# Optimization experiments

Hardware: AMD Instinct MI355X
Metric: run time of the kernel (lower is better)

Reference implementation:

```python
import jax, jax.numpy as jnp
import numpy as np

N_BITS = 8
QMAX = 2 ** (N_BITS - 1) - 1  # 127 for int8 symmetric
EPS = 1e-8


def fake_quant(x, axis):
    """Symmetric per-slice (row/col) dynamic fake quantization with STE-compatible form."""
    amax = jnp.max(jnp.abs(x), axis=axis, keepdims=True)
    scale = jnp.maximum(amax, EPS) / QMAX
    q = jnp.clip(jnp.round(x / scale), -QMAX - 1, QMAX) * scale
    return q


def setup_inputs() -> dict:
    key = jax.random.key(0)
    k1, k2 = jax.random.split(key)
    inputs1 = jax.random.normal(k1, (2, 16, 2048, 128), dtype=jnp.float32)
    inputs2 = jax.random.normal(k2, (2, 16, 128, 2048), dtype=jnp.float32)
    return {"inputs1": inputs1, "inputs2": inputs2}


def reference(inputs1, inputs2):
    # input1: row-wise (axes=-1) quant; input2: axes=-1 (module default); output: row-wise
    q1 = fake_quant(inputs1, axis=-1)
    q2 = fake_quant(inputs2, axis=-1)
    out = jnp.matmul(q1, q2)  # [B, H, S, S]
    return fake_quant(out, axis=-1)
```

## Files before the change

### kernel.cpp

```cpp
#include <hip/hip_runtime.h>
#include <hip/hip_bf16.h>
#include <cstdint>

#define QMAXF 127.0f
#define EPSQ 1e-8f

typedef __bf16 bf16x8 __attribute__((ext_vector_type(8)));
typedef float f32x4 __attribute__((ext_vector_type(4)));

static constexpr int BB = 32;
static constexpr int MM = 2048;
static constexpr int KK = 128;
static constexpr int NN = 2048;

static constexpr size_t OFF_Q1   = 0;
static constexpr size_t OFF_Q2T  = OFF_Q1  + (size_t)BB*MM*KK*2;
static constexpr size_t OFF_S1   = OFF_Q2T + (size_t)BB*NN*KK*2;
static constexpr size_t OFF_S2   = OFF_S1  + (size_t)BB*MM*4;

__global__ __launch_bounds__(256) void quant_rows128(const float* __restrict__ x,
                                                     unsigned short* __restrict__ q,
                                                     float* __restrict__ s1) {
    int wave = threadIdx.x >> 6, lane = threadIdx.x & 63;
    int row = blockIdx.x * 4 + wave;
    const float2* xr = reinterpret_cast<const float2*>(x) + (size_t)row * 64;
    float2 v = xr[lane];
    float a = fmaxf(fabsf(v.x), fabsf(v.y));
#pragma unroll
    for (int m = 32; m; m >>= 1) a = fmaxf(a, __shfl_xor(a, m));
    float scale = fmaxf(a, EPSQ) / QMAXF;
    float i0 = fminf(fmaxf(rintf(v.x / scale), -128.f), 127.f);
    float i1 = fminf(fmaxf(rintf(v.y / scale), -128.f), 127.f);
    __bf16 h0 = (__bf16)i0, h1 = (__bf16)i1;
    ushort2 st;
    st.x = *reinterpret_cast<unsigned short*>(&h0);
    st.y = *reinterpret_cast<unsigned short*>(&h1);
    reinterpret_cast<ushort2*>(q + (size_t)row * 128)[lane ^ ((row & 7) << 2)] = st;
    if (lane == 0) s1[row] = scale;
}

__global__ __launch_bounds__(256) void amax_rows2048(const float* __restrict__ x,
                                                     float* __restrict__ s2) {
    int row = blockIdx.x;
    const float4* xr = reinterpret_cast<const float4*>(x) + (size_t)row * 512;
    int t = threadIdx.x;
    float4 v0 = xr[t], v1 = xr[t + 256];
    float a = fmaxf(fmaxf(fmaxf(fabsf(v0.x), fabsf(v0.y)), fmaxf(fabsf(v0.z), fabsf(v0.w))),
                    fmaxf(fmaxf(fabsf(v1.x), fabsf(v1.y)), fmaxf(fabsf(v1.z), fabsf(v1.w))));
#pragma unroll
    for (int m = 32; m; m >>= 1) a = fmaxf(a, __shfl_xor(a, m));
    __shared__ float red[4];
    if ((t & 63) == 0) red[t >> 6] = a;
    __syncthreads();
    if (t == 0) {
        float m0 = fmaxf(fmaxf(red[0], red[1]), fmaxf(red[2], red[3]));
        s2[row] = fmaxf(m0, EPSQ) / QMAXF;
    }
}

__global__ __launch_bounds__(256) void quant_transpose(const float* __restrict__ x,
                                                       const float* __restrict__ s2,
                                                       unsigned short* __restrict__ q2t) {
    int b = blockIdx.x >> 5;
    int n0 = (blockIdx.x & 31) * 64;
    __shared__ unsigned short lds[64][136];
    int t = threadIdx.x;
    int rr = t >> 4, cc = t & 15;
#pragma unroll
    for (int p = 0; p < 8; ++p) {
        int k = p * 16 + rr;
        float s = s2[b * 128 + k];
        const float4* src = reinterpret_cast<const float4*>(x + ((size_t)b * 128 + k) * 2048 + n0);
        float4 v = src[cc];
        float f[4] = {v.x, v.y, v.z, v.w};
#pragma unroll
        for (int e = 0; e < 4; ++e) {
            float iq = fminf(fmaxf(rintf(f[e] / s), -128.f), 127.f);
            __bf16 h = (__bf16)(iq * s);
            lds[cc * 4 + e][k] = *reinterpret_cast<unsigned short*>(&h);
        }
    }
    __syncthreads();
    int nl = t >> 2, seg = t & 3;
    int sw = nl & 7;
    uint4* dstrow = reinterpret_cast<uint4*>(q2t + ((size_t)b * 2048 + n0 + nl) * 128);
#pragma unroll
    for (int j = 0; j < 4; ++j)
        dstrow[(seg * 4 + j) ^ sw] = *reinterpret_cast<const uint4*>(&lds[nl][seg * 32 + j * 8]);
}

__global__ __launch_bounds__(256, 2) void gemm_fused(const unsigned short* __restrict__ qa,
                                                     const unsigned short* __restrict__ qbt,
                                                     const float* __restrict__ s1,
                                                     float* __restrict__ out) {
    int id = blockIdx.x;
    int nid = (id & 7) * 64 + (id >> 3);
    int b = nid >> 4, mt = nid & 15;

    __shared__ float rowAmax[128], sOsc[128], sQs[128], sS1[128];

    int tid = threadIdx.x, wave = tid >> 6, lane = tid & 63;
    if (tid < 128) {
        rowAmax[tid] = 0.f;
        sS1[tid] = s1[b * 2048 + mt * 128 + tid];
    }

    int wm = wave >> 1, wn = wave & 1;
    int lr = lane & 15, lg = lane >> 4;
    int swz = (lr & 7) << 3;

    bf16x8 afr[4][4];
    {
        const unsigned short* Ai = qa + (size_t)(b * 16 + mt) * 16384;
#pragma unroll
        for (int ks = 0; ks < 4; ++ks)
#pragma unroll
            for (int mi = 0; mi < 4; ++mi)
                afr[ks][mi] = *reinterpret_cast<const bf16x8*>(
                    &Ai[(wm * 64 + mi * 16 + lr) * 128 + ((ks * 32 + lg * 8) ^ swz)]);
    }

    const unsigned short* Bimg = qbt + (size_t)b * 16 * 16384;
    auto boff = [&](int nt, int ks, int ni) -> size_t {
        return (size_t)(nt * 128 + wn * 64 + ni * 16 + lr) * 128 + ((ks * 32 + lg * 8) ^ swz);
    };

    bf16x8 bfr[4][4];
#pragma unroll
    for (int ks = 0; ks < 4; ++ks)
#pragma unroll
        for (int ni = 0; ni < 4; ++ni)
            bfr[ks][ni] = *reinterpret_cast<const bf16x8*>(&Bimg[boff(0, ks, ni)]);

    size_t ob = (size_t)b * 2048 * 2048;
    float rmax[4] = {0.f, 0.f, 0.f, 0.f};

    for (int nt = 0; nt < 16; ++nt) {
        int nn = (nt + 1) & 15;
        f32x4 acc[4][4];
#pragma unroll
        for (int mi = 0; mi < 4; ++mi)
#pragma unroll
            for (int ni = 0; ni < 4; ++ni) {
                f32x4 z = {0.f, 0.f, 0.f, 0.f};
                acc[mi][ni] = z;
            }
#pragma unroll
        for (int ks = 0; ks < 4; ++ks) {
#pragma unroll
            for (int mi = 0; mi < 4; ++mi)
#pragma unroll
                for (int ni = 0; ni < 4; ++ni)
                    acc[mi][ni] = __builtin_amdgcn_mfma_f32_16x16x32_bf16(bfr[ks][ni], afr[ks][mi], acc[mi][ni], 0, 0, 0);
#pragma unroll
            for (int ni = 0; ni < 4; ++ni)
                bfr[ks][ni] = *reinterpret_cast<const bf16x8*>(&Bimg[boff(nn, ks, ni)]);
        }
#pragma unroll
        for (int mi = 0; mi < 4; ++mi)
#pragma unroll
            for (int ni = 0; ni < 4; ++ni)
#pragma unroll
                for (int r = 0; r < 4; ++r)
                    rmax[mi] = fmaxf(rmax[mi], fabsf(acc[mi][ni][r]));
    }

#pragma unroll
    for (int mi = 0; mi < 4; ++mi) {
        float v = rmax[mi];
        v = fmaxf(v, __shfl_xor(v, 16));
        v = fmaxf(v, __shfl_xor(v, 32));
        if (lg == 0) {
            int row = wm * 64 + mi * 16 + lr;
            atomicMax(reinterpret_cast<unsigned*>(&rowAmax[row]), __float_as_uint(v));
        }
    }
    __syncthreads();
    if (tid < 128) {
        float am = rowAmax[tid] * sS1[tid];
        float osc = fmaxf(am, EPSQ) / QMAXF;
        sOsc[tid] = osc;
        sQs[tid] = sS1[tid] / osc;
    }
    __syncthreads();

    for (int nt = 0; nt < 16; ++nt) {
        int nn = (nt + 1) & 15;
        f32x4 acc[4][4];
#pragma unroll
        for (int mi = 0; mi < 4; ++mi)
#pragma unroll
            for (int ni = 0; ni < 4; ++ni) {
                f32x4 z = {0.f, 0.f, 0.f, 0.f};
                acc[mi][ni] = z;
            }
#pragma unroll
        for (int ks = 0; ks < 4; ++ks) {
#pragma unroll
            for (int mi = 0; mi < 4; ++mi)
#pragma unroll
                for (int ni = 0; ni < 4; ++ni)
                    acc[mi][ni] = __builtin_amdgcn_mfma_f32_16x16x32_bf16(bfr[ks][ni], afr[ks][mi], acc[mi][ni], 0, 0, 0);
#pragma unroll
            for (int ni = 0; ni < 4; ++ni)
                bfr[ks][ni] = *reinterpret_cast<const bf16x8*>(&Bimg[boff(nn, ks, ni)]);
        }
#pragma unroll
        for (int mi = 0; mi < 4; ++mi) {
            int row = wm * 64 + mi * 16 + lr;
            float qs = sQs[row], osc = sOsc[row];
            size_t rowoff = ob + (size_t)(mt * 128 + row) * 2048 + nt * 128 + wn * 64 + lg * 4;
#pragma unroll
            for (int ni = 0; ni < 4; ++ni) {
                f32x4 qv;
                qv[0] = fminf(fmaxf(rintf(acc[mi][ni][0] * qs), -128.f), 127.f) * osc;
                qv[1] = fminf(fmaxf(rintf(acc[mi][ni][1] * qs), -128.f), 127.f) * osc;
                qv[2] = fminf(fmaxf(rintf(acc[mi][ni][2] * qs), -128.f), 127.f) * osc;
                qv[3] = fminf(fmaxf(rintf(acc[mi][ni][3] * qs), -128.f), 127.f) * osc;
                *reinterpret_cast<f32x4*>(&out[rowoff + ni * 16]) = qv;
            }
        }
    }
}

extern "C" void kernel_launch(void* const* d_in, const int* in_sizes, int n_in,
                              void* d_out, int out_size, void* d_ws, size_t ws_size,
                              hipStream_t stream) {
    const float* in1 = (const float*)d_in[0];
    const float* in2 = (const float*)d_in[1];
    char* ws = (char*)d_ws;
    unsigned short* q1  = (unsigned short*)(ws + OFF_Q1);
    unsigned short* q2t = (unsigned short*)(ws + OFF_Q2T);
    float* s1   = (float*)(ws + OFF_S1);
    float* s2   = (float*)(ws + OFF_S2);
    float* out  = (float*)d_out;

    quant_rows128 <<<BB * MM / 4, 256, 0, stream>>>(in1, q1, s1);
    amax_rows2048 <<<BB * KK,     256, 0, stream>>>(in2, s2);
    quant_transpose<<<BB * (NN / 64), 256, 0, stream>>>(in2, s2, q2t);
    gemm_fused    <<<BB * 16,     256, 0, stream>>>(q1, q2t, s1, out);
}
```

Before: 191.8 us.

## Re-tile fused GEMM so each wave covers all 128 rows and prefetches B four tiles ahead

Changes the fused quantized GEMM's wave decomposition. Each wave now holds A fragments for all 128 rows and one 16-column strip per 64-column step, instead of a 64x64 quadrant. B is loaded through four rotating register banks, so each load is issued four sub-tiles ahead to hide global-load latency. The per-row scale and inverse are packed into one float2 in LDS. The cost is doubled A-fragment registers and narrower per-wave output writes (16 columns per store group), which may cost occupancy or store coalescing.

```diff
diff --git a/kernel.cpp b/kernel.cpp
--- a/kernel.cpp
+++ b/kernel.cpp
@@ -97,129 +97,121 @@
     int nid = (id & 7) * 64 + (id >> 3);
     int b = nid >> 4, mt = nid & 15;
 
-    __shared__ float rowAmax[128], sOsc[128], sQs[128], sS1[128];
+    __shared__ float rowAmax[128], sS1[128];
+    __shared__ float2 sQO[128];
 
     int tid = threadIdx.x, wave = tid >> 6, lane = tid & 63;
     if (tid < 128) {
         rowAmax[tid] = 0.f;
         sS1[tid] = s1[b * 2048 + mt * 128 + tid];
     }
-
-    int wm = wave >> 1, wn = wave & 1;
+    __syncthreads();
+
     int lr = lane & 15, lg = lane >> 4;
     int swz = (lr & 7) << 3;
 
-    bf16x8 afr[4][4];
+    bf16x8 afr[4][8];
     {
         const unsigned short* Ai = qa + (size_t)(b * 16 + mt) * 16384;
 #pragma unroll
         for (int ks = 0; ks < 4; ++ks)
 #pragma unroll
-            for (int mi = 0; mi < 4; ++mi)
+            for (int mi = 0; mi < 8; ++mi)
                 afr[ks][mi] = *reinterpret_cast<const bf16x8*>(
-                    &Ai[(wm * 64 + mi * 16 + lr) * 128 + ((ks * 32 + lg * 8) ^ swz)]);
+                    &Ai[(mi * 16 + lr) * 128 + ((ks * 32 + lg * 8) ^ swz)]);
     }
 
     const unsigned short* Bimg = qbt + (size_t)b * 16 * 16384;
-    auto boff = [&](int nt, int ks, int ni) -> size_t {
-        return (size_t)(nt * 128 + wn * 64 + ni * 16 + lr) * 128 + ((ks * 32 + lg * 8) ^ swz);
+    auto boff = [&](int t64, int ks) -> size_t {
+        return (size_t)(t64 * 64 + wave * 16 + lr) * 128 + ((ks * 32 + lg * 8) ^ swz);
     };
 
-    bf16x8 bfr[4][4];
-#pragma unroll
-    for (int ks = 0; ks < 4; ++ks)
-#pragma unroll
-        for (int ni = 0; ni < 4; ++ni)
-            bfr[ks][ni] = *reinterpret_cast<const bf16x8*>(&Bimg[boff(0, ks, ni)]);
+    bf16x8 bk0[4], bk1[4], bk2[4], bk3[4];
+#pragma unroll
+    for (int ks = 0; ks < 4; ++ks) {
+        bk0[ks] = *reinterpret_cast<const bf16x8*>(&Bimg[boff(0, ks)]);
+        bk1[ks] = *reinterpret_cast<const bf16x8*>(&Bimg[boff(1, ks)]);
+        bk2[ks] = *reinterpret_cast<const bf16x8*>(&Bimg[boff(2, ks)]);
+        bk3[ks] = *reinterpret_cast<const bf16x8*>(&Bimg[boff(3, ks)]);
+    }
 
     size_t ob = (size_t)b * 2048 * 2048;
-    float rmax[4] = {0.f, 0.f, 0.f, 0.f};
-
-    for (int nt = 0; nt < 16; ++nt) {
-        int nn = (nt + 1) & 15;
-        f32x4 acc[4][4];
-#pragma unroll
-        for (int mi = 0; mi < 4; ++mi)
-#pragma unroll
-            for (int ni = 0; ni < 4; ++ni) {
-                f32x4 z = {0.f, 0.f, 0.f, 0.f};
-                acc[mi][ni] = z;
-            }
+    float rmax[8];
+#pragma unroll
+    for (int mi = 0; mi < 8; ++mi) rmax[mi] = 0.f;
+
+    auto s1body = [&](int t, bf16x8 (&bank)[4]) {
+        f32x4 acc[8];
+#pragma unroll
+        for (int mi = 0; mi < 8; ++mi) { f32x4 z = {0.f,0.f,0.f,0.f}; acc[mi] = z; }
+        int nn = (t + 4) & 31;
 #pragma unroll
         for (int ks = 0; ks < 4; ++ks) {
 #pragma unroll
-            for (int mi = 0; mi < 4; ++mi)
-#pragma unroll
-                for (int ni = 0; ni < 4; ++ni)
-                    acc[mi][ni] = __builtin_amdgcn_mfma_f32_16x16x32_bf16(bfr[ks][ni], afr[ks][mi], acc[mi][ni], 0, 0, 0);
-#pragma unroll
-            for (int ni = 0; ni < 4; ++ni)
-                bfr[ks][ni] = *reinterpret_cast<const bf16x8*>(&Bimg[boff(nn, ks, ni)]);
-        }
-#pragma unroll
-        for (int mi = 0; mi < 4; ++mi)
-#pragma unroll
-            for (int ni = 0; ni < 4; ++ni)
-#pragma unroll
-                for (int r = 0; r < 4; ++r)
-                    rmax[mi] = fmaxf(rmax[mi], fabsf(acc[mi][ni][r]));
-    }
-
-#pragma unroll
-    for (int mi = 0; mi < 4; ++mi) {
+            for (int mi = 0; mi < 8; ++mi)
+                acc[mi] = __builtin_amdgcn_mfma_f32_16x16x32_bf16(bank[ks], afr[ks][mi], acc[mi], 0, 0, 0);
+            bank[ks] = *reinterpret_cast<const bf16x8*>(&Bimg[boff(nn, ks)]);
+        }
+#pragma unroll
+        for (int mi = 0; mi < 8; ++mi)
+#pragma unroll
+            for (int r = 0; r < 4; ++r)
+                rmax[mi] = fmaxf(rmax[mi], fabsf(acc[mi][r]));
+    };
+    for (int t = 0; t < 32; t += 4) {
+        s1body(t + 0, bk0);
+        s1body(t + 1, bk1);
+        s1body(t + 2, bk2);
+        s1body(t + 3, bk3);
+    }
+
+#pragma unroll
+    for (int mi = 0; mi < 8; ++mi) {
         float v = rmax[mi];
         v = fmaxf(v, __shfl_xor(v, 16));
         v = fmaxf(v, __shfl_xor(v, 32));
         if (lg == 0) {
-            int row = wm * 64 + mi * 16 + lr;
-            atomicMax(reinterpret_cast<unsigned*>(&rowAmax[row]), __float_as_uint(v));
+            atomicMax(reinterpret_cast<unsigned*>(&rowAmax[mi * 16 + lr]), __float_as_uint(v));
         }
     }
     __syncthreads();
     if (tid < 128) {
         float am = rowAmax[tid] * sS1[tid];
         float osc = fmaxf(am, EPSQ) / QMAXF;
-        sOsc[tid] = osc;
-        sQs[tid] = sS1[tid] / osc;
-    }
-    __syncthreads();
-
-    for (int nt = 0; nt < 16; ++nt) {
-        int nn = (nt + 1) & 15;
-        f32x4 acc[4][4];
-#pragma unroll
-        for (int mi = 0; mi < 4; ++mi)
-#pragma unroll
-            for (int ni = 0; ni < 4; ++ni) {
-                f32x4 z = {0.f, 0.f, 0.f, 0.f};
-                acc[mi][ni] = z;
-            }
+        sQO[tid] = make_float2(sS1[tid] / osc, osc);
+    }
+    __syncthreads();
+
+    auto s2body = [&](int t, bf16x8 (&bank)[4]) {
+        f32x4 acc[8];
+#pragma unroll
+        for (int mi = 0; mi < 8; ++mi) { f32x4 z = {0.f,0.f,0.f,0.f}; acc[mi] = z; }
+        int nn = (t + 4) & 31;
 #pragma unroll
         for (int ks = 0; ks < 4; ++ks) {
 #pragma unroll
-            for (int mi = 0; mi < 4; ++mi)
-#pragma unroll
-                for (int ni = 0; ni < 4; ++ni)
-                    acc[mi][ni] = __builtin_amdgcn_mfma_f32_16x16x32_bf16(bfr[ks][ni], afr[ks][mi], acc[mi][ni], 0, 0, 0);
-#pragma unroll
-            for (int ni = 0; ni < 4; ++ni)
-                bfr[ks][ni] = *reinterpret_cast<const bf16x8*>(&Bimg[boff(nn, ks, ni)]);
-        }
-#pragma unroll
-        for (int mi = 0; mi < 4; ++mi) {
-            int row = wm * 64 + mi * 16 + lr;
-            float qs = sQs[row], osc = sOsc[row];
-            size_t rowoff = ob + (size_t)(mt * 128 + row) * 2048 + nt * 128 + wn * 64 + lg * 4;
-#pragma unroll
-            for (int ni = 0; ni < 4; ++ni) {
-                f32x4 qv;
-                qv[0] = fminf(fmaxf(rintf(acc[mi][ni][0] * qs), -128.f), 127.f) * osc;
-                qv[1] = fminf(fmaxf(rintf(acc[mi][ni][1] * qs), -128.f), 127.f) * osc;
-                qv[2] = fminf(fmaxf(rintf(acc[mi][ni][2] * qs), -128.f), 127.f) * osc;
-                qv[3] = fminf(fmaxf(rintf(acc[mi][ni][3] * qs), -128.f), 127.f) * osc;
-                *reinterpret_cast<f32x4*>(&out[rowoff + ni * 16]) = qv;
-            }
-        }
+            for (int mi = 0; mi < 8; ++mi)
+                acc[mi] = __builtin_amdgcn_mfma_f32_16x16x32_bf16(bank[ks], afr[ks][mi], acc[mi], 0, 0, 0);
+            bank[ks] = *reinterpret_cast<const bf16x8*>(&Bimg[boff(nn, ks)]);
+        }
+#pragma unroll
+        for (int mi = 0; mi < 8; ++mi) {
+            int row = mi * 16 + lr;
+            float2 qo = sQO[row];
+            f32x4 qv;
+            qv[0] = fminf(fmaxf(rintf(acc[mi][0] * qo.x), -128.f), 127.f) * qo.y;
+            qv[1] = fminf(fmaxf(rintf(acc[mi][1] * qo.x), -128.f), 127.f) * qo.y;
+            qv[2] = fminf(fmaxf(rintf(acc[mi][2] * qo.x), -128.f), 127.f) * qo.y;
+            qv[3] = fminf(fmaxf(rintf(acc[mi][3] * qo.x), -128.f), 127.f) * qo.y;
+            *reinterpret_cast<f32x4*>(
+                &out[ob + (size_t)(mt * 128 + row) * 2048 + t * 64 + wave * 16 + lg * 4]) = qv;
+        }
+    };
+    for (int t = 0; t < 32; t += 4) {
+        s2body(t + 0, bk0);
+        s2body(t + 1, bk1);
+        s2body(t + 2, bk2);
+        s2body(t + 3, bk3);
     }
 }
 
```

New measurement: 535.7 us. +179.2%, slower.
